# Optimization experiments

Hardware: AMD Instinct MI355X
Metric: run time of the kernel (lower is better)

## Reference

```python
import jax, jax.numpy as jnp
import numpy as np

LN_EPS = 1e-5  # torch nn.LayerNorm default


def setup_inputs() -> dict:
    key = jax.random.key(0)
    ks = jax.random.split(key, 5)
    B, N, K, H, D = 1, 16384, 16, 4, 32
    q = jax.random.normal(ks[0], (B, N, H, D), dtype=jnp.float32)
    k_neigh = jax.random.normal(ks[1], (B, N, K, H, D), dtype=jnp.float32)
    v_neigh = jax.random.normal(ks[2], (B, N, K, H, D), dtype=jnp.float32)
    geo_f = jax.random.normal(ks[3], (B, N, K, D), dtype=jnp.float32)
    W = jax.random.normal(ks[4], (D, D), dtype=jnp.float32) * (1.0 / np.sqrt(D))
    b = jnp.zeros((D,), dtype=jnp.float32)
    ln_gamma = jnp.ones((D,), dtype=jnp.float32)
    ln_beta = jnp.zeros((D,), dtype=jnp.float32)
    return {"q": q, "k_neigh": k_neigh, "v_neigh": v_neigh, "geo_f": geo_f,
            "W": W, "b": b, "ln_gamma": ln_gamma, "ln_beta": ln_beta}


def reference(q, k_neigh, v_neigh, geo_f, W, b, ln_gamma, ln_beta):
    # q: [B,N,H,D], k_neigh/v_neigh: [B,N,K,H,D], geo_f: [B,N,K,D]
    scale = q.shape[-1] ** (-0.5)
    # broadcasted edge tensor [B,N,K,H,D]
    w = (q[:, :, None, :, :] - k_neigh + geo_f[:, :, :, None, :]) / scale
    # Linear(hdim,hdim) + ReLU + LayerNorm(hdim)
    w = jnp.einsum('bnkhd,ed->bnkhe', w, W) + b
    w = jax.nn.relu(w)
    mu = jnp.mean(w, axis=-1, keepdims=True)
    var = jnp.mean(jnp.square(w - mu), axis=-1, keepdims=True)
    w = (w - mu) * jax.lax.rsqrt(var + LN_EPS) * ln_gamma + ln_beta
    # subtract detached per-neighbor max (shift-invariant for softmax)
    w = w - jax.lax.stop_gradient(jnp.max(w, axis=2, keepdims=True))
    attn = jax.nn.softmax(w, axis=2)  # softmax over K neighbors
    # dropout p=0.0 -> identity
    out = jnp.sum(attn * v_neigh, axis=2)  # [B,N,H,D]
    return out
```

## Files before the change

### kernel.cpp

```cpp
#include <hip/hip_runtime.h>
#include <hip/hip_bf16.h>

constexpr int KNB = 16;
constexpr int HH  = 4;
constexpr int DD  = 32;
constexpr int NPB = 16;

typedef __attribute__((ext_vector_type(4))) float f32x4;
typedef __attribute__((ext_vector_type(8))) short bf16x8;
union BFRAG { bf16x8 v; unsigned u[4]; };

constexpr int L_K  = 0;
constexpr int L_V  = 2048;
constexpr int L_G  = 4096;
constexpr int L_Q  = 4608;
constexpr int L_SZ = 4864;

__device__ __forceinline__ unsigned pk_bf16(float a, float b) {
    union { __hip_bfloat162 b2; unsigned u; } r;
    r.b2 = __float22bfloat162_rn(make_float2(a, b));
    return r.u;
}
__device__ __forceinline__ float2 unpk_bf16(unsigned u) {
    union { unsigned u; __hip_bfloat162 b2; } r; r.u = u;
    return make_float2(__bfloat162float(r.b2.x), __bfloat162float(r.b2.y));
}
__device__ __forceinline__ void gload16(const float* g, float* l) {
    __builtin_amdgcn_global_load_lds(
        (const __attribute__((address_space(1))) unsigned*)g,
        (__attribute__((address_space(3))) unsigned*)l, 16, 0, 0);
}

__global__ __launch_bounds__(256, 4) void geoneigh_pipe(
    const float* __restrict__ q, const float* __restrict__ kn,
    const float* __restrict__ vn, const float* __restrict__ geo,
    const float* __restrict__ W, const float* __restrict__ bvec,
    const float* __restrict__ gamma, const float* __restrict__ beta,
    float* __restrict__ out, int BN)
{
    __shared__ __align__(16) float lds[2][L_SZ];

    const int tid = threadIdx.x;
    const int l   = tid & 63;
    const int wv  = tid >> 6;
    const int lm  = l & 15;
    const int lg  = l >> 4;

    const float SC    = 5.656854249492381f;
    const float LOG2E = 1.4426950408889634f;

    BFRAG Wh[2], Wl[2];
    #pragma unroll
    for (int t = 0; t < 2; ++t) {
        const float* wr = &W[(t * 16 + lm) * DD + lg * 8];
        const float4 wa = *(const float4*)wr;
        const float4 wb = *(const float4*)(wr + 4);
        float wf[8] = {wa.x * SC, wa.y * SC, wa.z * SC, wa.w * SC,
                       wb.x * SC, wb.y * SC, wb.z * SC, wb.w * SC};
        #pragma unroll
        for (int p = 0; p < 4; ++p) {
            const unsigned h = pk_bf16(wf[2 * p], wf[2 * p + 1]);
            const float2 hr = unpk_bf16(h);
            Wh[t].u[p] = h;
            Wl[t].u[p] = pk_bf16(wf[2 * p] - hr.x, wf[2 * p + 1] - hr.y);
        }
    }
    float bias[2], gamL[2], betL[2];
    #pragma unroll
    for (int t = 0; t < 2; ++t) {
        bias[t] = bvec[lm + 16 * t];
        gamL[t] = gamma[lm + 16 * t] * LOG2E;
        betL[t] = beta[lm + 16 * t] * LOG2E;
    }

    const int koff0 = lm * 128 + wv * 32 + lg * 8;
    const int vbase = (((l >> 2) & 3) * 4 + wv) * 128 + lg * 32 + (l & 3) * 4;
    const int goff  = lm * 32 + lg * 8 + (wv & 1) * 4;
    const int qoff  = (l & 31) * 4;
    const int dK = L_K + 2 * wv * 256;
    const int dV = L_V + 2 * wv * 256;
    const int dG = L_G + (wv & 1) * 256;

    const int nbase = blockIdx.x * NPB;
    const int nmax  = BN - 1;

    auto stage = [&](int buf, int n) {
        const float* kN = kn  + (size_t)n * (KNB * HH * DD);
        const float* vN = vn  + (size_t)n * (KNB * HH * DD);
        const float* gN = geo + (size_t)n * (KNB * DD);
        const float* qN = q   + (size_t)n * (HH * DD);
        float* B = &lds[buf][0];
        gload16(kN + koff0,      B + dK);
        gload16(kN + koff0 + 4,  B + dK + 256);
        gload16(vN + vbase,      B + dV);
        gload16(vN + vbase + 16, B + dV + 256);
        gload16(gN + goff,       B + dG);
        gload16(qN + qoff,       B + L_Q);
    };
    auto cnode = [&](int t) { int n = nbase + t; return n > nmax ? nmax : n; };

    stage(0, cnode(0));

    #pragma unroll 2
    for (int t = 0; t < NPB; ++t) {
        stage((t + 1) & 1, cnode(t + 1));
        asm volatile("s_waitcnt vmcnt(6)" ::: "memory");
        __builtin_amdgcn_s_barrier();
        __builtin_amdgcn_sched_barrier(0);

        const float* B = &lds[t & 1][0];
        const int n = cnode(t);

        const f32x4 kf0 = *(const f32x4*)(B + L_K + wv * 512 + l * 4);
        const f32x4 kf1 = *(const f32x4*)(B + L_K + wv * 512 + 256 + l * 4);
        const f32x4 gf0 = *(const f32x4*)(B + L_G + l * 4);
        const f32x4 gf1 = *(const f32x4*)(B + L_G + 256 + l * 4);
        const f32x4 qf0 = *(const f32x4*)(B + L_Q + wv * 32 + lg * 8);
        const f32x4 qf1 = *(const f32x4*)(B + L_Q + wv * 32 + lg * 8 + 4);
        float vr[2][4];
        #pragma unroll
        for (int t2 = 0; t2 < 2; ++t2)
            #pragma unroll
            for (int r = 0; r < 4; ++r)
                vr[t2][r] = B[L_V + (r * 32 + t2 * 16 + wv * 4 + lg) * 16 + lm];

        float wvv[8];
        #pragma unroll
        for (int j = 0; j < 4; ++j) {
            wvv[j]     = qf0[j] - kf0[j] + gf0[j];
            wvv[4 + j] = qf1[j] - kf1[j] + gf1[j];
        }
        BFRAG Ah, Al;
        #pragma unroll
        for (int p = 0; p < 4; ++p) {
            const unsigned h = pk_bf16(wvv[2 * p], wvv[2 * p + 1]);
            const float2 hr = unpk_bf16(h);
            Ah.u[p] = h;
            Al.u[p] = pk_bf16(wvv[2 * p] - hr.x, wvv[2 * p + 1] - hr.y);
        }
        f32x4 acc[2];
        #pragma unroll
        for (int t2 = 0; t2 < 2; ++t2) {
            f32x4 c = {bias[t2], bias[t2], bias[t2], bias[t2]};
            c = __builtin_amdgcn_mfma_f32_16x16x32_bf16(Ah.v, Wh[t2].v, c, 0, 0, 0);
            c = __builtin_amdgcn_mfma_f32_16x16x32_bf16(Ah.v, Wl[t2].v, c, 0, 0, 0);
            c = __builtin_amdgcn_mfma_f32_16x16x32_bf16(Al.v, Wh[t2].v, c, 0, 0, 0);
            acc[t2] = c;
        }

        float x[2][4], t1[4], t2s[4];
        #pragma unroll
        for (int t2 = 0; t2 < 2; ++t2)
            #pragma unroll
            for (int r = 0; r < 4; ++r)
                x[t2][r] = fmaxf(acc[t2][r], 0.f);
        #pragma unroll
        for (int r = 0; r < 4; ++r) {
            t1[r]  = x[0][r] + x[1][r];
            t2s[r] = x[0][r] * x[0][r] + x[1][r] * x[1][r];
        }
        #pragma unroll
        for (int m = 1; m <= 8; m <<= 1) {
            #pragma unroll
            for (int r = 0; r < 4; ++r) {
                t1[r]  += __shfl_xor(t1[r], m);
                t2s[r] += __shfl_xor(t2s[r], m);
            }
        }
        float z[2][4];
        #pragma unroll
        for (int r = 0; r < 4; ++r) {
            const float mu  = t1[r] * 0.03125f;
            const float var = fmaxf(t2s[r] * 0.03125f - mu * mu, 0.f);
            const float inv = rsqrtf(var + 1e-5f);
            #pragma unroll
            for (int t2 = 0; t2 < 2; ++t2)
                z[t2][r] = (x[t2][r] - mu) * inv * gamL[t2] + betL[t2];
        }
        float S[2], o[2];
        #pragma unroll
        for (int t2 = 0; t2 < 2; ++t2) {
            float s = 0.f, oo = 0.f;
            #pragma unroll
            for (int r = 0; r < 4; ++r) {
                const float p = exp2f(z[t2][r]);
                s += p;
                oo = fmaf(p, vr[t2][r], oo);
            }
            s  += __shfl_xor(s, 16);
            s  += __shfl_xor(s, 32);
            oo += __shfl_xor(oo, 16);
            oo += __shfl_xor(oo, 32);
            S[t2] = s; o[t2] = oo;
        }
        if (l < 32) {
            const int sel = (l >> 4) & 1;
            const float oo = sel ? o[1] : o[0];
            const float ss = sel ? S[1] : S[0];
            out[((size_t)n * HH + wv) * DD + l] = __fdividef(oo, ss);
        }

        asm volatile("s_waitcnt lgkmcnt(0)" ::: "memory");
        __builtin_amdgcn_s_barrier();
    }
}

extern "C" void kernel_launch(void* const* d_in, const int* in_sizes, int n_in,
                              void* d_out, int out_size, void* d_ws, size_t ws_size,
                              hipStream_t stream) {
    const float* q   = (const float*)d_in[0];
    const float* kn  = (const float*)d_in[1];
    const float* vn  = (const float*)d_in[2];
    const float* geo = (const float*)d_in[3];
    const float* W   = (const float*)d_in[4];
    const float* b   = (const float*)d_in[5];
    const float* gam = (const float*)d_in[6];
    const float* bet = (const float*)d_in[7];
    float* out = (float*)d_out;

    const int BN     = in_sizes[0] / (HH * DD);
    const int blocks = (BN + NPB - 1) / NPB;

    hipLaunchKernelGGL(geoneigh_pipe, dim3(blocks), dim3(256), 0, stream,
                       q, kn, vn, geo, W, b, gam, bet, out, BN);
}
```

Measured before the change: 68.77 us.

## Deepen LDS prefetch to triple buffering, relayout V staging, use DPP reductions

Replaces double buffering with a three-deep ring of LDS buffers, prefetching two nodes ahead with vmcnt(12). This is meant to hide more global-load latency in a memory-bound kernel. It doubles nodes per block and lowers launch_bounds occupancy from 4 to 2. It also changes the V staging layout so lane reads are contiguous, and replaces the first two shuffle steps of the LayerNorm reduction with DPP swaps. The cost is more LDS per block and fewer resident blocks, which may offset the gain from the deeper pipeline.

```diff
diff --git a/kernel.cpp b/kernel.cpp
--- a/kernel.cpp
+++ b/kernel.cpp
@@ -4,7 +4,8 @@
 constexpr int KNB = 16;
 constexpr int HH  = 4;
 constexpr int DD  = 32;
-constexpr int NPB = 16;
+constexpr int NPB = 32;
+constexpr int NBUF = 3;
 
 typedef __attribute__((ext_vector_type(4))) float f32x4;
 typedef __attribute__((ext_vector_type(8))) short bf16x8;
@@ -30,15 +31,25 @@
         (const __attribute__((address_space(1))) unsigned*)g,
         (__attribute__((address_space(3))) unsigned*)l, 16, 0, 0);
 }
-
-__global__ __launch_bounds__(256, 4) void geoneigh_pipe(
+__device__ __forceinline__ float dpp_x1(float x) {
+    int s = __builtin_bit_cast(int, x);
+    return __builtin_bit_cast(float,
+        __builtin_amdgcn_update_dpp(s, s, 0xB1, 0xF, 0xF, false));
+}
+__device__ __forceinline__ float dpp_x2(float x) {
+    int s = __builtin_bit_cast(int, x);
+    return __builtin_bit_cast(float,
+        __builtin_amdgcn_update_dpp(s, s, 0x4E, 0xF, 0xF, false));
+}
+
+__global__ __launch_bounds__(256, 2) void geoneigh_deep(
     const float* __restrict__ q, const float* __restrict__ kn,
     const float* __restrict__ vn, const float* __restrict__ geo,
     const float* __restrict__ W, const float* __restrict__ bvec,
     const float* __restrict__ gamma, const float* __restrict__ beta,
     float* __restrict__ out, int BN)
 {
-    __shared__ __align__(16) float lds[2][L_SZ];
+    __shared__ __align__(16) float lds[NBUF * L_SZ];
 
     const int tid = threadIdx.x;
     const int l   = tid & 63;
@@ -74,11 +85,12 @@
     }
 
     const int koff0 = lm * 128 + wv * 32 + lg * 8;
-    const int vbase = (((l >> 2) & 3) * 4 + wv) * 128 + lg * 32 + (l & 3) * 4;
+    const int voff  = ((l >> 2) & 3) * 512 + wv * 128
+                    + ((l >> 4) & 3) * 32 + (l & 3) * 4;
     const int goff  = lm * 32 + lg * 8 + (wv & 1) * 4;
     const int qoff  = (l & 31) * 4;
-    const int dK = L_K + 2 * wv * 256;
-    const int dV = L_V + 2 * wv * 256;
+    const int dK = L_K + wv * 512;
+    const int dV = L_V + wv * 512;
     const int dG = L_G + (wv & 1) * 256;
 
     const int nbase = blockIdx.x * NPB;
@@ -89,26 +101,28 @@
         const float* vN = vn  + (size_t)n * (KNB * HH * DD);
         const float* gN = geo + (size_t)n * (KNB * DD);
         const float* qN = q   + (size_t)n * (HH * DD);
-        float* B = &lds[buf][0];
+        float* B = &lds[buf * L_SZ];
         gload16(kN + koff0,      B + dK);
         gload16(kN + koff0 + 4,  B + dK + 256);
-        gload16(vN + vbase,      B + dV);
-        gload16(vN + vbase + 16, B + dV + 256);
+        gload16(vN + voff,       B + dV);
+        gload16(vN + voff + 16,  B + dV + 256);
         gload16(gN + goff,       B + dG);
         gload16(qN + qoff,       B + L_Q);
+        __builtin_amdgcn_sched_barrier(0);
     };
     auto cnode = [&](int t) { int n = nbase + t; return n > nmax ? nmax : n; };
 
     stage(0, cnode(0));
-
-    #pragma unroll 2
+    stage(1, cnode(1));
+
+    int cb = 0, sb = 2;
     for (int t = 0; t < NPB; ++t) {
-        stage((t + 1) & 1, cnode(t + 1));
-        asm volatile("s_waitcnt vmcnt(6)" ::: "memory");
+        stage(sb, cnode(t + 2));
+        asm volatile("s_waitcnt vmcnt(12)" ::: "memory");
         __builtin_amdgcn_s_barrier();
         __builtin_amdgcn_sched_barrier(0);
 
-        const float* B = &lds[t & 1][0];
+        const float* B = &lds[cb * L_SZ];
         const int n = cnode(t);
 
         const f32x4 kf0 = *(const f32x4*)(B + L_K + wv * 512 + l * 4);
@@ -122,7 +136,7 @@
         for (int t2 = 0; t2 < 2; ++t2)
             #pragma unroll
             for (int r = 0; r < 4; ++r)
-                vr[t2][r] = B[L_V + (r * 32 + t2 * 16 + wv * 4 + lg) * 16 + lm];
+                vr[t2][r] = B[L_V + (r * 2 + t2) * 256 + wv * 64 + l];
 
         float wvv[8];
         #pragma unroll
@@ -160,12 +174,11 @@
             t2s[r] = x[0][r] * x[0][r] + x[1][r] * x[1][r];
         }
         #pragma unroll
-        for (int m = 1; m <= 8; m <<= 1) {
-            #pragma unroll
-            for (int r = 0; r < 4; ++r) {
-                t1[r]  += __shfl_xor(t1[r], m);
-                t2s[r] += __shfl_xor(t2s[r], m);
-            }
+        for (int r = 0; r < 4; ++r) {
+            t1[r]  += dpp_x1(t1[r]);   t2s[r] += dpp_x1(t2s[r]);
+            t1[r]  += dpp_x2(t1[r]);   t2s[r] += dpp_x2(t2s[r]);
+            t1[r]  += __shfl_xor(t1[r], 4);  t2s[r] += __shfl_xor(t2s[r], 4);
+            t1[r]  += __shfl_xor(t1[r], 8);  t2s[r] += __shfl_xor(t2s[r], 8);
         }
         float z[2][4];
         #pragma unroll
@@ -202,6 +215,8 @@
 
         asm volatile("s_waitcnt lgkmcnt(0)" ::: "memory");
         __builtin_amdgcn_s_barrier();
+        cb = (cb == NBUF - 1) ? 0 : cb + 1;
+        sb = (sb == NBUF - 1) ? 0 : sb + 1;
     }
 }
 
@@ -221,6 +236,6 @@
     const int BN     = in_sizes[0] / (HH * DD);
     const int blocks = (BN + NPB - 1) / NPB;
 
-    hipLaunchKernelGGL(geoneigh_pipe, dim3(blocks), dim3(256), 0, stream,
+    hipLaunchKernelGGL(geoneigh_deep, dim3(blocks), dim3(256), 0, stream,
                        q, kn, vn, geo, W, b, gam, bet, out, BN);
 }
```

New measurement: 71.34 us. 1.04x slower.
